# Kernel tuning notes

Measured on AMD Instinct MI355X. Metric: run time of the kernel, lower is better.

## Reference

```python
import jax, jax.numpy as jnp
import numpy as np

T, N, C, S = 1024, 128, 256, 64  # time, batch, classes, max label len
BLANK = 0
NEG = -1e30  # effective -inf that keeps logaddexp grads finite


def setup_inputs() -> dict:
    key = jax.random.key(0)
    k1, k2, k3 = jax.random.split(key, 3)
    logits = jax.random.normal(k1, (T, N, C), dtype=jnp.float32)
    y = jax.random.randint(k2, (N, S), 1, C)          # labels in [1, C), blank=0
    ylens = jax.random.randint(k3, (N, 1), 16, S + 1)  # 2*ylen+1 <= T always
    xlens = jnp.full((N, 1), T, dtype=jnp.int32)
    return {"logits": logits, "y": y, "xlens": xlens, "ylens": ylens}


def _ctc_loss(log_probs, y, xl, yl):
    """Standard CTC forward DP (alpha recursion), mean reduction, zero_infinity."""
    Tt, Nn, Cc = log_probs.shape
    Ss = y.shape[1]
    L = 2 * Ss + 1
    # extended label sequence: blank, y1, blank, y2, ..., blank
    ext = jnp.zeros((Nn, L), dtype=y.dtype).at[:, 1::2].set(y)
    # skip transition (s-2 -> s) allowed iff ext[s] != blank and ext[s] != ext[s-2]
    allow_skip = jnp.concatenate(
        [jnp.zeros((Nn, 2), bool),
         (ext[:, 2:] != ext[:, :-2]) & (ext[:, 2:] != BLANK)], axis=1)
    # gather per-time log-probs of extended labels: (T, N, L)
    lp_ext = jnp.take_along_axis(
        log_probs, jnp.broadcast_to(ext[None], (Tt, Nn, L)), axis=2)

    alpha0 = (jnp.full((Nn, L), NEG, jnp.float32)
              .at[:, 0].set(lp_ext[0, :, 0])
              .at[:, 1].set(lp_ext[0, :, 1]))

    def step(alpha, inp):
        lp_t, t = inp
        a1 = jnp.concatenate([jnp.full((Nn, 1), NEG, alpha.dtype), alpha[:, :-1]], axis=1)
        a2 = jnp.concatenate([jnp.full((Nn, 2), NEG, alpha.dtype), alpha[:, :-2]], axis=1)
        a2 = jnp.where(allow_skip, a2, NEG)
        new = lp_t + jnp.logaddexp(jnp.logaddexp(alpha, a1), a2)
        alpha = jnp.where((t < xl)[:, None], new, alpha)  # freeze past xlen
        return alpha, None

    alpha, _ = jax.lax.scan(step, alpha0, (lp_ext[1:], jnp.arange(1, Tt)))

    end = 2 * yl  # index of last blank in extended sequence
    la = jnp.take_along_axis(alpha, end[:, None], axis=1)[:, 0]
    lb = jnp.take_along_axis(alpha, (end - 1)[:, None], axis=1)[:, 0]
    nll = -jnp.logaddexp(la, lb)
    nll = jnp.where(jnp.isfinite(nll) & (nll < 1e29), nll, 0.0)  # zero_infinity
    return jnp.mean(nll / yl)  # reduction='mean': divide by target length, avg over batch


def reference(logits, y, xlens, ylens):
    log_probs = jax.nn.log_softmax(logits, axis=-1)
    return _ctc_loss(log_probs, y, xlens.reshape(-1), ylens.reshape(-1))
```

## Files before the change

kernel.cpp:

```cpp
#include <hip/hip_runtime.h>
#include <math.h>

constexpr int kT = 1024;
constexpr int kN = 128;
constexpr int kC = 256;
constexpr float NEGV = -1e30f;
constexpr int kRow = 260;
constexpr int kRowB = kRow * 4;
constexpr int kCH = 32;
constexpr int kNCH = 512 / kCH;
constexpr int kChF = 8 * kRow;
constexpr int kChB = kChF * 4;
constexpr float LOG2E = 1.4426950408889634f;
constexpr float LN2 = 0.6931471805599453f;

#if __has_builtin(__builtin_amdgcn_exp2f)
#define EXP2(x) __builtin_amdgcn_exp2f(x)
#else
#define EXP2(x) exp2f(x)
#endif
#if __has_builtin(__builtin_amdgcn_logf)
#define LOG2(x) __builtin_amdgcn_logf(x)
#else
#define LOG2(x) log2f(x)
#endif

struct TrueT { static constexpr bool value = true; };
struct FalseT { static constexpr bool value = false; };

__device__ __forceinline__ float lse2_2(float a, float b) {
    const float m = fmaxf(a, b);
    const float d = fminf(a, b) - m;
    return m + LOG2(1.0f + EXP2(d));
}

__device__ __forceinline__ float lse2_e(float a, float b) {
    const float m = fmaxf(a, b);
    return m + __logf(1.0f + __expf(fminf(a, b) - m));
}

__device__ __forceinline__ float lse3_e(float a, float b, float c) {
    const float m = fmaxf(fmaxf(a, b), c);
    return m + __logf(__expf(a - m) + __expf(b - m) + __expf(c - m));
}

template <bool GATHER>
__global__ __launch_bounds__(256) void k_lse(const float* __restrict__ logits,
                                             const int* __restrict__ y,
                                             float* __restrict__ lpg,
                                             float* __restrict__ lse_out) {
    __shared__ float srow[4][kC];
    __shared__ float sT[4][65];
    const int w = threadIdx.x >> 6;
    const int lane = threadIdx.x & 63;
    const int n = blockIdx.x & (kN - 1);
    const int t4 = blockIdx.x >> 7;
    const int t = t4 * 4 + w;
    const int row = t * kN + n;

    const float4 v = reinterpret_cast<const float4*>(logits + (size_t)row * kC)[lane];
    float m = fmaxf(fmaxf(v.x, v.y), fmaxf(v.z, v.w));
#pragma unroll
    for (int o = 32; o > 0; o >>= 1) m = fmaxf(m, __shfl_xor(m, o));
    float s = __expf(v.x - m) + __expf(v.y - m) + __expf(v.z - m) + __expf(v.w - m);
#pragma unroll
    for (int o = 32; o > 0; o >>= 1) s += __shfl_xor(s, o);

    if (GATHER) {
        const float log2s = LOG2(s);
        float* sr = srow[w];
        reinterpret_cast<float4*>(sr)[lane] = v;
        const int cls = y[(n << 6) + lane];
        sT[w][1 + lane] = (sr[cls] - m) * LOG2E - log2s;
        if (lane == 0) sT[w][0] = (v.x - m) * LOG2E - log2s;
        __syncthreads();
        float* op = lpg + (size_t)n * (kT / 4) * kRow + (size_t)t4 * kRow;
        const int tid = threadIdx.x;
        op[tid] = sT[tid & 3][tid >> 2];
        if (tid < 4) op[256 + tid] = sT[tid][64];
    } else {
        if (lane == 0) lse_out[row] = m + __logf(s);
    }
}

template <bool FRZ>
__device__ __forceinline__ void dp_step(float& A, float& B, float& C,
                                        float lpb, float lpy, bool skip,
                                        int lgrp, int l, bool commit) {
    const int bi = __float_as_int(B);
    const int b15 = __builtin_amdgcn_readlane(bi, 15);
    const int b31 = __builtin_amdgcn_readlane(bi, 31);
    const int b47 = __builtin_amdgcn_readlane(bi, 47);
    const int b63 = __builtin_amdgcn_readlane(bi, 63);
    const int bndi = (lgrp == 0) ? b63 : (lgrp == 1) ? b15 : (lgrp == 2) ? b31 : b47;
    const float am1 = __int_as_float(__builtin_amdgcn_update_dpp(
        bndi, bi, 0x111 , 0xF, 0xF, false));
    const float am1s = skip ? am1 : NEGV;
    const float x = fmaxf(B, A), yv = fminf(B, A);
    const float mB = fmaxf(x, am1s);
    const float dB1 = fmaxf(yv, fminf(x, am1s)) - mB;
    const float dB2 = fminf(yv, am1s) - mB;
    const float nB = (lpy + mB) + LOG2(1.0f + (EXP2(dB1) + EXP2(dB2)));
    const float u = (l == 0) ? C : A;
    const float mA = fmaxf(u, am1);
    const float lseA = mA + LOG2(1.0f + EXP2(fminf(u, am1) - mA));
    const float nA = lpb + ((l == 0) ? A : lseA);
    const float nC = lpb + lseA;
    if (FRZ) {
        A = commit ? nA : A;
        B = commit ? nB : B;
        C = commit ? nC : C;
    } else {
        A = nA; B = nB; C = nC;
    }
}

__global__ __launch_bounds__(512) void k_dp_split(const float* __restrict__ lpg,
                                                  const int* __restrict__ y,
                                                  const int* __restrict__ xlens,
                                                  const int* __restrict__ ylens,
                                                  float* __restrict__ nll_out) {
    __shared__ alignas(16) float sbf[2][kChF];
    __shared__ alignas(16) float sbb[2][kChF];
    __shared__ float st_f[130];
    __shared__ float st_b[130];
    const int n = blockIdx.x;
    const int wid = threadIdx.x >> 6;
    const int l = threadIdx.x & 63;
    const int lgrp = l >> 4;
    const char* src = (const char*)(lpg + (size_t)n * (kT / 4) * kRow);

    auto stage = [&](int c, int b, bool isF) {
        const int widx = isF ? (wid - 2) : (wid - 5);
        const long off = isF ? (long)c * kChB : (long)(256 - 8 * (c + 1)) * kRowB;
        const char* gs = src + off;
        char* ls = (char*)(isF ? &sbf[b][0] : &sbb[b][0]);
#pragma unroll
        for (int r = 0; r < 3; ++r) {
            const int wi = widx * 64 + r * 192;
            if (wi + l < kChB / 16) {
                __builtin_amdgcn_global_load_lds(
                    (const __attribute__((address_space(1))) void*)(gs + (size_t)(wi + l) * 16),
                    (__attribute__((address_space(3))) void*)(ls + (size_t)wi * 16), 16, 0, 0);
            }
        }
    };

    if (wid >= 2) stage(0, 0, wid < 5);
    __syncthreads();

    const int yl = ylens[n];
    const int xl = xlens[n];

    if (wid == 0) {
        const int ycur = y[(n << 6) + l];
        const int yprev = __shfl_up(ycur, 1);
        const bool skip = (l >= 1) && (ycur != yprev);
        float aA = (l == 0) ? sbf[0][0] : NEGV;
        float aB = (l == 0) ? sbf[0][4] : NEGV;
        float aC = NEGV;

        for (int c = 0; c < kNCH; ++c) {
            const float* B = sbf[c & 1];
            const int tb0 = c * kCH;
            auto body = [&](auto frzc) {
                constexpr bool FRZV = decltype(frzc)::value;
                float pb[2][4][4], py[2][4][4];
#define LOADF(H, D)                                                          \
    do {                                                                     \
        _Pragma("unroll") for (int q_ = 0; q_ < 4; ++q_) {                   \
            const int rb_ = (4 * (H) + q_) * kRow;                           \
            const float4 t0_ = *(const float4*)&B[rb_];                      \
            const float4 t1_ = *(const float4*)&B[rb_ + 4 + 4 * l];          \
            pb[D][q_][0] = t0_.x; pb[D][q_][1] = t0_.y;                      \
            pb[D][q_][2] = t0_.z; pb[D][q_][3] = t0_.w;                      \
            py[D][q_][0] = t1_.x; py[D][q_][1] = t1_.y;                      \
            py[D][q_][2] = t1_.z; py[D][q_][3] = t1_.w;                      \
        }                                                                    \
    } while (0)
                LOADF(0, 0);
#pragma unroll
                for (int h = 0; h < 2; ++h) {
                    const int cur = h & 1, nxt = cur ^ 1;
                    if (h < 1) LOADF(1, 1);
#pragma unroll
                    for (int q = 0; q < 4; ++q) {
#pragma unroll
                        for (int j = 0; j < 4; ++j) {
                            const int t = tb0 + 16 * h + 4 * q + j;
                            dp_step<FRZV>(aA, aB, aC, pb[cur][q][j], py[cur][q][j],
                                          skip, lgrp, l, (t > 0) & (t < xl));
                        }
                    }
                }
#undef LOADF
            };
            if (c == 0 || xl < 512) body(TrueT{});
            else body(FalseT{});
            __syncthreads();
        }
        st_f[2 * l] = aA;
        st_f[2 * l + 1] = aB;
        if (l == 0) st_f[128] = aC;
        __syncthreads();

        const float v0 = st_f[l] + st_b[l];
        const float v1 = st_f[64 + l] + st_b[64 + l];
        const float v2 = (l == 0) ? (st_f[128] + st_b[128]) : NEGV;
        float mm = fmaxf(fmaxf(v0, v1), v2);
#pragma unroll
        for (int o = 32; o > 0; o >>= 1) mm = fmaxf(mm, __shfl_xor(mm, o));
        float sm = EXP2(v0 - mm) + EXP2(v1 - mm) + EXP2(v2 - mm);
#pragma unroll
        for (int o = 32; o > 0; o >>= 1) sm += __shfl_xor(sm, o);
        if (l == 0) {
            float nll;
            if (xl <= 512) {
                nll = -lse2_2(st_f[2 * yl], st_f[2 * yl - 1]) * LN2;
            } else {
                nll = -(mm + LOG2(sm)) * LN2;
            }
            if (!(isfinite(nll) && nll < 1e29f)) nll = 0.0f;
            nll_out[n] = nll / (float)yl;
        }
    } else if (wid == 1) {
        const int ycb = y[(n << 6) + 63 - l];
        const int yup = __shfl_up(ycb, 1);
        const bool skipb = (l >= 1) && (ycb != yup);
        const int ls = 64 - yl;
        float bA = NEGV, bB = NEGV, b0 = NEGV;

        for (int c = 0; c < kNCH; ++c) {
            const float* B = sbb[c & 1];
            const int ttop = 1023 - kCH * c;
            auto body = [&](auto frzc) {
                constexpr bool FRZV = decltype(frzc)::value;
                float pb[2][4][4], py[2][4][4];
#define LOADB(H, D)                                                          \
    do {                                                                     \
        _Pragma("unroll") for (int q_ = 0; q_ < 4; ++q_) {                   \
            const int rb_ = (7 - 4 * (H) - q_) * kRow;                       \
            const float4 t0_ = *(const float4*)&B[rb_];                      \
            const float4 t1_ = *(const float4*)&B[rb_ + 256 - 4 * l];        \
            pb[D][q_][0] = t0_.x; pb[D][q_][1] = t0_.y;                      \
            pb[D][q_][2] = t0_.z; pb[D][q_][3] = t0_.w;                      \
            py[D][q_][0] = t1_.x; py[D][q_][1] = t1_.y;                      \
            py[D][q_][2] = t1_.z; py[D][q_][3] = t1_.w;                      \
        }                                                                    \
    } while (0)
                LOADB(0, 0);
#pragma unroll
                for (int h = 0; h < 2; ++h) {
                    const int cur = h & 1, nxt = cur ^ 1;
                    if (h < 1) LOADB(1, 1);
#pragma unroll
                    for (int q = 0; q < 4; ++q) {
#pragma unroll
                        for (int jr = 0; jr < 4; ++jr) {
                            const int j = 3 - jr;
                            const int t = ttop - (16 * h + 4 * q + jr);
                            const float lpb = pb[cur][q][j];
                            const float lpy = py[cur][q][j];
                            dp_step<FRZV>(bA, bB, b0, lpb, lpy, skipb, lgrp, l,
                                          (t >= 512) & (t <= xl - 2));
                            if (FRZV) {
                                const bool ss = (t == xl - 1);
                                bA = ss ? ((l == ls) ? lpb : NEGV) : bA;
                                bB = ss ? ((l == ls) ? lpy : NEGV) : bB;
                                b0 = ss ? NEGV : b0;
                            }
                        }
                    }
                }
#undef LOADB
            };
            if (c == 0 || xl < kT) body(TrueT{});
            else body(FalseT{});
            __syncthreads();
        }
        dp_step<false>(bA, bB, b0, 0.0f, 0.0f, skipb, lgrp, l, true);
        st_b[128 - 2 * l] = bA;
        st_b[127 - 2 * l] = bB;
        if (l == 0) st_b[0] = b0;
        __syncthreads();
    } else {
        for (int c = 0; c < kNCH; ++c) {
            if (c + 1 < kNCH) stage(c + 1, (c + 1) & 1, wid < 5);
            __syncthreads();
        }
        __syncthreads();
    }
}

template <int PFB>
__global__ __launch_bounds__(64) void k_dp_fb(const float* __restrict__ logits,
                                              const float* __restrict__ lsearr,
                                              const int* __restrict__ y,
                                              const int* __restrict__ xlens,
                                              const int* __restrict__ ylens,
                                              float* __restrict__ nll_out) {
    const int n = blockIdx.x;
    const int l = threadIdx.x;
    const int yl = ylens[n];
    const int xl = xlens[n];
    const int ycur = y[(n << 6) + l];
    const int yprev = __shfl_up(ycur, 1);
    const bool skip = (l >= 1) && (ycur != yprev);

    auto load_lp = [&](int t, float& lpb, float& lpy) {
        const float* p = logits + ((size_t)t * kN + n) * kC;
        const float d = lsearr[t * kN + n];
        lpb = p[0] - d;
        lpy = p[ycur] - d;
    };

    float lpb0, lpy0;
    load_lp(0, lpb0, lpy0);
    float aA = (l == 0) ? lpb0 : NEGV;
    float aB = (l == 0) ? lpy0 : NEGV;
    float aC = NEGV;

    float pb[PFB], py[PFB];
#pragma unroll
    for (int k = 0; k < PFB; ++k) load_lp(1 + k, pb[k], py[k]);

    for (int tb = 1; tb < kT; tb += PFB) {
#pragma unroll
        for (int k = 0; k < PFB; ++k) {
            const int t = tb + k;
            if (t < kT) {
                const float lpb = pb[k], lpy = py[k];
                if (t + PFB < kT) load_lp(t + PFB, pb[k], py[k]);
                float am1 = __shfl_up(aB, 1);
                if (l == 0) am1 = NEGV;
                const float nA = lpb + lse2_e(aA, am1);
                const float nB = lpy + lse3_e(aB, aA, skip ? am1 : NEGV);
                float nC = aC;
                if (l == 63) nC = lpb + lse2_e(aC, aB);
                if (t < xl) { aA = nA; aB = nB; aC = nC; }
            }
        }
    }

    __shared__ float st[130];
    st[2 * l] = aA;
    st[2 * l + 1] = aB;
    if (l == 63) st[128] = aC;
    __syncthreads();
    if (l == 0) {
        const int end = 2 * yl;
        float nll = -lse2_e(st[end], st[end - 1]);
        if (!(isfinite(nll) && nll < 1e29f)) nll = 0.0f;
        nll_out[n] = nll / (float)yl;
    }
}

__global__ __launch_bounds__(128) void k_reduce(const float* __restrict__ nll,
                                                float* __restrict__ out) {
    const int tid = threadIdx.x;
    float v = nll[tid];
#pragma unroll
    for (int o = 32; o > 0; o >>= 1) v += __shfl_xor(v, o);
    __shared__ float partial[2];
    if ((tid & 63) == 0) partial[tid >> 6] = v;
    __syncthreads();
    if (tid == 0) out[0] = (partial[0] + partial[1]) * (1.0f / (float)kN);
}

extern "C" void kernel_launch(void* const* d_in, const int* in_sizes, int n_in,
                              void* d_out, int out_size, void* d_ws, size_t ws_size,
                              hipStream_t stream) {
    const float* logits = (const float*)d_in[0];
    const int* y = (const int*)d_in[1];
    const int* xlens = (const int*)d_in[2];
    const int* ylens = (const int*)d_in[3];
    float* out = (float*)d_out;

    const size_t need_full =
        (size_t)kN * (kT / 4) * kRow * sizeof(float) + kN * sizeof(float);
    const int rows = kT * kN;

    if (ws_size >= need_full) {
        float* lpg = (float*)d_ws;
        float* nll = lpg + (size_t)kN * (kT / 4) * kRow;
        k_lse<true><<<rows / 4, 256, 0, stream>>>(logits, y, lpg, nullptr);
        k_dp_split<<<kN, 512, 0, stream>>>(lpg, y, xlens, ylens, nll);
        k_reduce<<<1, kN, 0, stream>>>(nll, out);
    } else {
        float* lsearr = (float*)d_ws;
        float* nll = lsearr + (size_t)rows;
        k_lse<false><<<rows / 4, 256, 0, stream>>>(logits, y, nullptr, lsearr);
        k_dp_fb<8><<<kN, 64, 0, stream>>>(logits, lsearr, y, xlens, ylens, nll);
        k_reduce<<<1, kN, 0, stream>>>(nll, out);
    }
}
```

Baseline: 96.20 us.

## Fuse log-softmax gather into DP kernel producer warps

Removes the separate log-softmax/gather kernel and its workspace intermediate; producer warps in the DP kernel now load logits rows directly, compute the row max and sum via wave shuffles, gather the label log-probs through shared scratch, and write them into the double-buffered LDS chunks. This avoids a kernel launch and a global write/read of the gathered array. The trade-off is that all logits traffic now comes from only 128 blocks, which may cut achievable bandwidth, and the producer compute must keep pace with the serial DP warps. The low-workspace fallback path is dropped.

```diff
diff --git a/kernel.cpp b/kernel.cpp
--- a/kernel.cpp
+++ b/kernel.cpp
@@ -6,11 +6,9 @@
 constexpr int kC = 256;
 constexpr float NEGV = -1e30f;
 constexpr int kRow = 260;
-constexpr int kRowB = kRow * 4;
 constexpr int kCH = 32;
 constexpr int kNCH = 512 / kCH;
 constexpr int kChF = 8 * kRow;
-constexpr int kChB = kChF * 4;
 constexpr float LOG2E = 1.4426950408889634f;
 constexpr float LN2 = 0.6931471805599453f;
 
@@ -32,55 +30,6 @@
     const float m = fmaxf(a, b);
     const float d = fminf(a, b) - m;
     return m + LOG2(1.0f + EXP2(d));
-}
-
-__device__ __forceinline__ float lse2_e(float a, float b) {
-    const float m = fmaxf(a, b);
-    return m + __logf(1.0f + __expf(fminf(a, b) - m));
-}
-
-__device__ __forceinline__ float lse3_e(float a, float b, float c) {
-    const float m = fmaxf(fmaxf(a, b), c);
-    return m + __logf(__expf(a - m) + __expf(b - m) + __expf(c - m));
-}
-
-template <bool GATHER>
-__global__ __launch_bounds__(256) void k_lse(const float* __restrict__ logits,
-                                             const int* __restrict__ y,
-                                             float* __restrict__ lpg,
-                                             float* __restrict__ lse_out) {
-    __shared__ float srow[4][kC];
-    __shared__ float sT[4][65];
-    const int w = threadIdx.x >> 6;
-    const int lane = threadIdx.x & 63;
-    const int n = blockIdx.x & (kN - 1);
-    const int t4 = blockIdx.x >> 7;
-    const int t = t4 * 4 + w;
-    const int row = t * kN + n;
-
-    const float4 v = reinterpret_cast<const float4*>(logits + (size_t)row * kC)[lane];
-    float m = fmaxf(fmaxf(v.x, v.y), fmaxf(v.z, v.w));
-#pragma unroll
-    for (int o = 32; o > 0; o >>= 1) m = fmaxf(m, __shfl_xor(m, o));
-    float s = __expf(v.x - m) + __expf(v.y - m) + __expf(v.z - m) + __expf(v.w - m);
-#pragma unroll
-    for (int o = 32; o > 0; o >>= 1) s += __shfl_xor(s, o);
-
-    if (GATHER) {
-        const float log2s = LOG2(s);
-        float* sr = srow[w];
-        reinterpret_cast<float4*>(sr)[lane] = v;
-        const int cls = y[(n << 6) + lane];
-        sT[w][1 + lane] = (sr[cls] - m) * LOG2E - log2s;
-        if (lane == 0) sT[w][0] = (v.x - m) * LOG2E - log2s;
-        __syncthreads();
-        float* op = lpg + (size_t)n * (kT / 4) * kRow + (size_t)t4 * kRow;
-        const int tid = threadIdx.x;
-        op[tid] = sT[tid & 3][tid >> 2];
-        if (tid < 4) op[256 + tid] = sT[tid][64];
-    } else {
-        if (lane == 0) lse_out[row] = m + __logf(s);
-    }
 }
 
 template <bool FRZ>
@@ -115,47 +64,74 @@
     }
 }
 
-__global__ __launch_bounds__(512) void k_dp_split(const float* __restrict__ lpg,
-                                                  const int* __restrict__ y,
-                                                  const int* __restrict__ xlens,
-                                                  const int* __restrict__ ylens,
-                                                  float* __restrict__ nll_out) {
+__global__ __launch_bounds__(512) void k_ctc_fused(const float* __restrict__ logits,
+                                                   const int* __restrict__ y,
+                                                   const int* __restrict__ xlens,
+                                                   const int* __restrict__ ylens,
+                                                   float* __restrict__ nll_out) {
     __shared__ alignas(16) float sbf[2][kChF];
     __shared__ alignas(16) float sbb[2][kChF];
+    __shared__ alignas(16) float scr[6][kC];
     __shared__ float st_f[130];
     __shared__ float st_b[130];
     const int n = blockIdx.x;
     const int wid = threadIdx.x >> 6;
     const int l = threadIdx.x & 63;
     const int lgrp = l >> 4;
-    const char* src = (const char*)(lpg + (size_t)n * (kT / 4) * kRow);
-
-    auto stage = [&](int c, int b, bool isF) {
-        const int widx = isF ? (wid - 2) : (wid - 5);
-        const long off = isF ? (long)c * kChB : (long)(256 - 8 * (c + 1)) * kRowB;
-        const char* gs = src + off;
-        char* ls = (char*)(isF ? &sbf[b][0] : &sbb[b][0]);
-#pragma unroll
-        for (int r = 0; r < 3; ++r) {
-            const int wi = widx * 64 + r * 192;
-            if (wi + l < kChB / 16) {
-                __builtin_amdgcn_global_load_lds(
-                    (const __attribute__((address_space(1))) void*)(gs + (size_t)(wi + l) * 16),
-                    (__attribute__((address_space(3))) void*)(ls + (size_t)wi * 16), 16, 0, 0);
-            }
-        }
-    };
-
-    if (wid >= 2) stage(0, 0, wid < 5);
-    __syncthreads();
 
     const int yl = ylens[n];
     const int xl = xlens[n];
+    const int cls = y[(n << 6) + l];
+
+    auto stage_sm = [&](int c, bool isF, float* dst) {
+        const int widx = isF ? (wid - 2) : (wid - 5);
+        const int scrw = wid - 2;
+        float4 v0, v1, v2, v3, v4, v5, v6, v7, v8, v9, v10;
+#define ROWT(K) (isF ? (c * kCH + widx + 3 * (K)) : (992 - kCH * c + widx + 3 * (K)))
+#define LOADR(K, V)                                                           \
+    do {                                                                      \
+        if (widx + 3 * (K) < kCH) {                                           \
+            const int tg_ = ROWT(K);                                          \
+            V = *reinterpret_cast<const float4*>(                             \
+                logits + ((size_t)tg_ * kN + n) * kC + 4 * l);                \
+        }                                                                     \
+    } while (0)
+        LOADR(0, v0); LOADR(1, v1); LOADR(2, v2); LOADR(3, v3);
+        LOADR(4, v4); LOADR(5, v5); LOADR(6, v6); LOADR(7, v7);
+        LOADR(8, v8); LOADR(9, v9); LOADR(10, v10);
+#define PROCR(K, V)                                                           \
+    do {                                                                      \
+        const int r_ = widx + 3 * (K);                                        \
+        if (r_ < kCH) {                                                       \
+            float m_ = fmaxf(fmaxf(V.x, V.y), fmaxf(V.z, V.w));               \
+            _Pragma("unroll") for (int o_ = 32; o_ > 0; o_ >>= 1)             \
+                m_ = fmaxf(m_, __shfl_xor(m_, o_));                           \
+            float s_ = __expf(V.x - m_) + __expf(V.y - m_) +                  \
+                       __expf(V.z - m_) + __expf(V.w - m_);                   \
+            _Pragma("unroll") for (int o_ = 32; o_ > 0; o_ >>= 1)             \
+                s_ += __shfl_xor(s_, o_);                                     \
+            const float l2s_ = LOG2(s_);                                      \
+            reinterpret_cast<float4*>(&scr[scrw][0])[l] = V;                  \
+            const float g_ = scr[scrw][cls];                                  \
+            const int t4_ = r_ >> 2, j_ = r_ & 3;                             \
+            dst[t4_ * kRow + (1 + l) * 4 + j_] = (g_ - m_) * LOG2E - l2s_;    \
+            if (l == 0) dst[t4_ * kRow + j_] = (V.x - m_) * LOG2E - l2s_;     \
+        }                                                                     \
+    } while (0)
+        PROCR(0, v0); PROCR(1, v1); PROCR(2, v2); PROCR(3, v3);
+        PROCR(4, v4); PROCR(5, v5); PROCR(6, v6); PROCR(7, v7);
+        PROCR(8, v8); PROCR(9, v9); PROCR(10, v10);
+#undef PROCR
+#undef LOADR
+#undef ROWT
+    };
+
+    if (wid >= 2) stage_sm(0, wid < 5, (wid < 5) ? sbf[0] : sbb[0]);
+    __syncthreads();
 
     if (wid == 0) {
-        const int ycur = y[(n << 6) + l];
-        const int yprev = __shfl_up(ycur, 1);
-        const bool skip = (l >= 1) && (ycur != yprev);
+        const int yprev = __shfl_up(cls, 1);
+        const bool skip = (l >= 1) && (cls != yprev);
         float aA = (l == 0) ? sbf[0][0] : NEGV;
         float aB = (l == 0) ? sbf[0][4] : NEGV;
         float aC = NEGV;
@@ -181,7 +157,7 @@
                 LOADF(0, 0);
 #pragma unroll
                 for (int h = 0; h < 2; ++h) {
-                    const int cur = h & 1, nxt = cur ^ 1;
+                    const int cur = h & 1;
                     if (h < 1) LOADF(1, 1);
 #pragma unroll
                     for (int q = 0; q < 4; ++q) {
@@ -251,7 +227,7 @@
                 LOADB(0, 0);
 #pragma unroll
                 for (int h = 0; h < 2; ++h) {
-                    const int cur = h & 1, nxt = cur ^ 1;
+                    const int cur = h & 1;
                     if (h < 1) LOADB(1, 1);
 #pragma unroll
                     for (int q = 0; q < 4; ++q) {
@@ -284,74 +260,13 @@
         if (l == 0) st_b[0] = b0;
         __syncthreads();
     } else {
+        const bool isF = wid < 5;
         for (int c = 0; c < kNCH; ++c) {
-            if (c + 1 < kNCH) stage(c + 1, (c + 1) & 1, wid < 5);
+            if (c + 1 < kNCH)
+                stage_sm(c + 1, isF, isF ? sbf[(c + 1) & 1] : sbb[(c + 1) & 1]);
             __syncthreads();
         }
         __syncthreads();
-    }
-}
-
-template <int PFB>
-__global__ __launch_bounds__(64) void k_dp_fb(const float* __restrict__ logits,
-                                              const float* __restrict__ lsearr,
-                                              const int* __restrict__ y,
-                                              const int* __restrict__ xlens,
-                                              const int* __restrict__ ylens,
-                                              float* __restrict__ nll_out) {
-    const int n = blockIdx.x;
-    const int l = threadIdx.x;
-    const int yl = ylens[n];
-    const int xl = xlens[n];
-    const int ycur = y[(n << 6) + l];
-    const int yprev = __shfl_up(ycur, 1);
-    const bool skip = (l >= 1) && (ycur != yprev);
-
-    auto load_lp = [&](int t, float& lpb, float& lpy) {
-        const float* p = logits + ((size_t)t * kN + n) * kC;
-        const float d = lsearr[t * kN + n];
-        lpb = p[0] - d;
-        lpy = p[ycur] - d;
-    };
-
-    float lpb0, lpy0;
-    load_lp(0, lpb0, lpy0);
-    float aA = (l == 0) ? lpb0 : NEGV;
-    float aB = (l == 0) ? lpy0 : NEGV;
-    float aC = NEGV;
-
-    float pb[PFB], py[PFB];
-#pragma unroll
-    for (int k = 0; k < PFB; ++k) load_lp(1 + k, pb[k], py[k]);
-
-    for (int tb = 1; tb < kT; tb += PFB) {
-#pragma unroll
-        for (int k = 0; k < PFB; ++k) {
-            const int t = tb + k;
-            if (t < kT) {
-                const float lpb = pb[k], lpy = py[k];
-                if (t + PFB < kT) load_lp(t + PFB, pb[k], py[k]);
-                float am1 = __shfl_up(aB, 1);
-                if (l == 0) am1 = NEGV;
-                const float nA = lpb + lse2_e(aA, am1);
-                const float nB = lpy + lse3_e(aB, aA, skip ? am1 : NEGV);
-                float nC = aC;
-                if (l == 63) nC = lpb + lse2_e(aC, aB);
-                if (t < xl) { aA = nA; aB = nB; aC = nC; }
-            }
-        }
-    }
-
-    __shared__ float st[130];
-    st[2 * l] = aA;
-    st[2 * l + 1] = aB;
-    if (l == 63) st[128] = aC;
-    __syncthreads();
-    if (l == 0) {
-        const int end = 2 * yl;
-        float nll = -lse2_e(st[end], st[end - 1]);
-        if (!(isfinite(nll) && nll < 1e29f)) nll = 0.0f;
-        nll_out[n] = nll / (float)yl;
     }
 }
 
@@ -376,21 +291,7 @@
     const int* ylens = (const int*)d_in[3];
     float* out = (float*)d_out;
 
-    const size_t need_full =
-        (size_t)kN * (kT / 4) * kRow * sizeof(float) + kN * sizeof(float);
-    const int rows = kT * kN;
-
-    if (ws_size >= need_full) {
-        float* lpg = (float*)d_ws;
-        float* nll = lpg + (size_t)kN * (kT / 4) * kRow;
-        k_lse<true><<<rows / 4, 256, 0, stream>>>(logits, y, lpg, nullptr);
-        k_dp_split<<<kN, 512, 0, stream>>>(lpg, y, xlens, ylens, nll);
-        k_reduce<<<1, kN, 0, stream>>>(nll, out);
-    } else {
-        float* lsearr = (float*)d_ws;
-        float* nll = lsearr + (size_t)rows;
-        k_lse<false><<<rows / 4, 256, 0, stream>>>(logits, y, nullptr, lsearr);
-        k_dp_fb<8><<<kN, 64, 0, stream>>>(logits, lsearr, y, xlens, ylens, nll);
-        k_reduce<<<1, kN, 0, stream>>>(nll, out);
-    }
-}
+    float* nll = (float*)d_ws;
+    k_ctc_fused<<<kN, 512, 0, stream>>>(logits, y, xlens, ylens, nll);
+    k_reduce<<<1, kN, 0, stream>>>(nll, out);
+}
```

After: 113.9 us. +18.4%, slower.

## Fuse two CTC DP time steps into one windowed transition per iteration

Applied to the files above, without the earlier changes.

The forward and backward alpha/beta recursions now advance two time steps per iteration in unfrozen chunks. A precomputed two-step transition (win_step) combines the log-probs of both steps into combined edge weights, so each pair of steps needs one log-sum-exp per state instead of two chained ones. This halves the serial dependency chain of DPP shifts and log/exp operations. In exchange it adds extra LDS loads for the neighbour's log-prob, more cross-lane shifts and more exp terms per step, and the rearranged sum order may change floating-point results slightly.

```diff
diff --git a/kernel.cpp b/kernel.cpp
--- a/kernel.cpp
+++ b/kernel.cpp
@@ -26,7 +26,6 @@
 #endif
 
 struct TrueT { static constexpr bool value = true; };
-struct FalseT { static constexpr bool value = false; };
 
 __device__ __forceinline__ float lse2_2(float a, float b) {
     const float m = fmaxf(a, b);
@@ -83,18 +82,21 @@
     }
 }
 
+__device__ __forceinline__ float row_shr1_b(float x, int lgrp) {
+    const int xi = __float_as_int(x);
+    const int b15 = __builtin_amdgcn_readlane(xi, 15);
+    const int b31 = __builtin_amdgcn_readlane(xi, 31);
+    const int b47 = __builtin_amdgcn_readlane(xi, 47);
+    const int b63 = __builtin_amdgcn_readlane(xi, 63);
+    const int bnd = (lgrp == 0) ? b63 : (lgrp == 1) ? b15 : (lgrp == 2) ? b31 : b47;
+    return __int_as_float(__builtin_amdgcn_update_dpp(bnd, xi, 0x111, 0xF, 0xF, false));
+}
+
 template <bool FRZ>
 __device__ __forceinline__ void dp_step(float& A, float& B, float& C,
                                         float lpb, float lpy, bool skip,
                                         int lgrp, int l, bool commit) {
-    const int bi = __float_as_int(B);
-    const int b15 = __builtin_amdgcn_readlane(bi, 15);
-    const int b31 = __builtin_amdgcn_readlane(bi, 31);
-    const int b47 = __builtin_amdgcn_readlane(bi, 47);
-    const int b63 = __builtin_amdgcn_readlane(bi, 63);
-    const int bndi = (lgrp == 0) ? b63 : (lgrp == 1) ? b15 : (lgrp == 2) ? b31 : b47;
-    const float am1 = __int_as_float(__builtin_amdgcn_update_dpp(
-        bndi, bi, 0x111 , 0xF, 0xF, false));
+    const float am1 = row_shr1_b(B, lgrp);
     const float am1s = skip ? am1 : NEGV;
     const float x = fmaxf(B, A), yv = fminf(B, A);
     const float mB = fmaxf(x, am1s);
@@ -115,6 +117,42 @@
     }
 }
 
+__device__ __forceinline__ void win_step(float& A, float& B, float& C,
+                                         float lpb0, float lpy0, float lpb1,
+                                         float lpy1, float lpy0m1, float skf,
+                                         float skm1f, float og2, float og4,
+                                         float e3g, int lgrp, int l) {
+    const float E0 = lpb0 + lpb1;
+    const float E1 = lpb1 + lse2_2(lpb0, lpy0m1);
+    const float E2 = lpb1 + lpy0m1;
+    const float E3 = E2 + skm1f + e3g;
+    const float O0 = lpy1 + lpy0;
+    const float O1 = lpy1 + lse2_2(lpy0, lpb0);
+    const float p0 = lpb0, p1 = skf + lpy0m1, p2 = skf + lpy0;
+    const float mx = fmaxf(fmaxf(p0, p1), p2);
+    const float md = fmaxf(fminf(p0, p1), fminf(fmaxf(p0, p1), p2));
+    const float mn = fminf(fminf(p0, p1), p2);
+    const float O2 = lpy1 + og2 + (mx + LOG2(1.0f + EXP2(md - mx) + EXP2(mn - mx)));
+    const float O3 = lpy1 + og2 + skf + lpy0m1;
+    const float O4 = lpy1 + og4 + skf + skm1f + lpy0m1;
+    const float s1A = row_shr1_b(A, lgrp);
+    const float s1B = row_shr1_b(B, lgrp);
+    const float s2B = row_shr1_b(s1B, lgrp);
+    const float u = (l == 0) ? C : A;
+    const float q0 = E0 + u, q1 = E1 + s1B, q2 = E2 + s1A, q3 = E3 + s2B;
+    const float mE = fmaxf(fmaxf(q0, q1), fmaxf(q2, q3));
+    const float sE = (EXP2(q0 - mE) + EXP2(q1 - mE)) + (EXP2(q2 - mE) + EXP2(q3 - mE));
+    const float lseE = mE + LOG2(sE);
+    const float nA = (l == 0) ? (E0 + A) : lseE;
+    const float nC = lseE;
+    const float r0 = O0 + B, r1 = O1 + A, r2 = O2 + s1B, r3 = O3 + s1A, r4 = O4 + s2B;
+    const float mO = fmaxf(fmaxf(fmaxf(r0, r1), fmaxf(r2, r3)), r4);
+    const float sO = (EXP2(r0 - mO) + EXP2(r1 - mO)) +
+                     (EXP2(r2 - mO) + EXP2(r3 - mO)) + EXP2(r4 - mO);
+    const float nB = mO + LOG2(sO);
+    A = nA; B = nB; C = nC;
+}
+
 __global__ __launch_bounds__(512) void k_dp_split(const float* __restrict__ lpg,
                                                   const int* __restrict__ y,
                                                   const int* __restrict__ xlens,
@@ -151,11 +189,18 @@
 
     const int yl = ylens[n];
     const int xl = xlens[n];
+    const float og2 = (l >= 1) ? 0.0f : NEGV;
+    const float og4 = (l >= 2) ? 0.0f : NEGV;
+    const float e3g = (l == 1) ? NEGV : 0.0f;
 
     if (wid == 0) {
         const int ycur = y[(n << 6) + l];
         const int yprev = __shfl_up(ycur, 1);
         const bool skip = (l >= 1) && (ycur != yprev);
+        const float skf = skip ? 0.0f : NEGV;
+        const float skm1f = __shfl(skf, (l + 63) & 63);
+        const int im1f = (l == 0) ? 256 : 4 * l;
+
         float aA = (l == 0) ? sbf[0][0] : NEGV;
         float aB = (l == 0) ? sbf[0][4] : NEGV;
         float aC = NEGV;
@@ -163,8 +208,7 @@
         for (int c = 0; c < kNCH; ++c) {
             const float* B = sbf[c & 1];
             const int tb0 = c * kCH;
-            auto body = [&](auto frzc) {
-                constexpr bool FRZV = decltype(frzc)::value;
+            if (c == 0 || tb0 + kCH - 1 >= xl) {
                 float pb[2][4][4], py[2][4][4];
 #define LOADF(H, D)                                                          \
     do {                                                                     \
@@ -181,22 +225,51 @@
                 LOADF(0, 0);
 #pragma unroll
                 for (int h = 0; h < 2; ++h) {
-                    const int cur = h & 1, nxt = cur ^ 1;
                     if (h < 1) LOADF(1, 1);
 #pragma unroll
                     for (int q = 0; q < 4; ++q) {
 #pragma unroll
                         for (int j = 0; j < 4; ++j) {
                             const int t = tb0 + 16 * h + 4 * q + j;
-                            dp_step<FRZV>(aA, aB, aC, pb[cur][q][j], py[cur][q][j],
+                            dp_step<true>(aA, aB, aC, pb[h][q][j], py[h][q][j],
                                           skip, lgrp, l, (t > 0) & (t < xl));
                         }
                     }
                 }
 #undef LOADF
-            };
-            if (c == 0 || xl < 512) body(TrueT{});
-            else body(FalseT{});
+            } else {
+                float pb[2][4][4], py[2][4][4], ph[2][4][4];
+#define LOADW(H, D)                                                          \
+    do {                                                                     \
+        _Pragma("unroll") for (int q_ = 0; q_ < 4; ++q_) {                   \
+            const int rb_ = (4 * (H) + q_) * kRow;                           \
+            const float4 t0_ = *(const float4*)&B[rb_];                      \
+            const float4 t1_ = *(const float4*)&B[rb_ + 4 + 4 * l];          \
+            const float4 t2_ = *(const float4*)&B[rb_ + im1f];               \
+            pb[D][q_][0] = t0_.x; pb[D][q_][1] = t0_.y;                      \
+            pb[D][q_][2] = t0_.z; pb[D][q_][3] = t0_.w;                      \
+            py[D][q_][0] = t1_.x; py[D][q_][1] = t1_.y;                      \
+            py[D][q_][2] = t1_.z; py[D][q_][3] = t1_.w;                      \
+            ph[D][q_][0] = t2_.x; ph[D][q_][1] = t2_.y;                      \
+            ph[D][q_][2] = t2_.z; ph[D][q_][3] = t2_.w;                      \
+        }                                                                    \
+    } while (0)
+                LOADW(0, 0);
+#pragma unroll
+                for (int h = 0; h < 2; ++h) {
+                    if (h < 1) LOADW(1, 1);
+#pragma unroll
+                    for (int q = 0; q < 4; ++q) {
+                        win_step(aA, aB, aC, pb[h][q][0], py[h][q][0],
+                                 pb[h][q][1], py[h][q][1], ph[h][q][0], skf,
+                                 skm1f, og2, og4, e3g, lgrp, l);
+                        win_step(aA, aB, aC, pb[h][q][2], py[h][q][2],
+                                 pb[h][q][3], py[h][q][3], ph[h][q][2], skf,
+                                 skm1f, og2, og4, e3g, lgrp, l);
+                    }
+                }
+#undef LOADW
+            }
             __syncthreads();
         }
         st_f[2 * l] = aA;
@@ -227,14 +300,16 @@
         const int ycb = y[(n << 6) + 63 - l];
         const int yup = __shfl_up(ycb, 1);
         const bool skipb = (l >= 1) && (ycb != yup);
+        const float skf = skipb ? 0.0f : NEGV;
+        const float skm1f = __shfl(skf, (l + 63) & 63);
+        const int im1b = (l == 0) ? 4 : 260 - 4 * l;
         const int ls = 64 - yl;
         float bA = NEGV, bB = NEGV, b0 = NEGV;
 
         for (int c = 0; c < kNCH; ++c) {
             const float* B = sbb[c & 1];
             const int ttop = 1023 - kCH * c;
-            auto body = [&](auto frzc) {
-                constexpr bool FRZV = decltype(frzc)::value;
+            if (ttop >= xl - 1) {
                 float pb[2][4][4], py[2][4][4];
 #define LOADB(H, D)                                                          \
     do {                                                                     \
@@ -251,7 +326,6 @@
                 LOADB(0, 0);
 #pragma unroll
                 for (int h = 0; h < 2; ++h) {
-                    const int cur = h & 1, nxt = cur ^ 1;
                     if (h < 1) LOADB(1, 1);
 #pragma unroll
                     for (int q = 0; q < 4; ++q) {
@@ -259,23 +333,51 @@
                         for (int jr = 0; jr < 4; ++jr) {
                             const int j = 3 - jr;
                             const int t = ttop - (16 * h + 4 * q + jr);
-                            const float lpb = pb[cur][q][j];
-                            const float lpy = py[cur][q][j];
-                            dp_step<FRZV>(bA, bB, b0, lpb, lpy, skipb, lgrp, l,
+                            const float lpb = pb[h][q][j];
+                            const float lpy = py[h][q][j];
+                            dp_step<true>(bA, bB, b0, lpb, lpy, skipb, lgrp, l,
                                           (t >= 512) & (t <= xl - 2));
-                            if (FRZV) {
-                                const bool ss = (t == xl - 1);
-                                bA = ss ? ((l == ls) ? lpb : NEGV) : bA;
-                                bB = ss ? ((l == ls) ? lpy : NEGV) : bB;
-                                b0 = ss ? NEGV : b0;
-                            }
+                            const bool ss = (t == xl - 1);
+                            bA = ss ? ((l == ls) ? lpb : NEGV) : bA;
+                            bB = ss ? ((l == ls) ? lpy : NEGV) : bB;
+                            b0 = ss ? NEGV : b0;
                         }
                     }
                 }
 #undef LOADB
-            };
-            if (c == 0 || xl < kT) body(TrueT{});
-            else body(FalseT{});
+            } else {
+                float pb[2][4][4], py[2][4][4], ph[2][4][4];
+#define LOADWB(H, D)                                                         \
+    do {                                                                     \
+        _Pragma("unroll") for (int q_ = 0; q_ < 4; ++q_) {                   \
+            const int rb_ = (7 - 4 * (H) - q_) * kRow;                       \
+            const float4 t0_ = *(const float4*)&B[rb_];                      \
+            const float4 t1_ = *(const float4*)&B[rb_ + 256 - 4 * l];        \
+            const float4 t2_ = *(const float4*)&B[rb_ + im1b];               \
+            pb[D][q_][0] = t0_.x; pb[D][q_][1] = t0_.y;                      \
+            pb[D][q_][2] = t0_.z; pb[D][q_][3] = t0_.w;                      \
+            py[D][q_][0] = t1_.x; py[D][q_][1] = t1_.y;                      \
+            py[D][q_][2] = t1_.z; py[D][q_][3] = t1_.w;                      \
+            ph[D][q_][0] = t2_.x; ph[D][q_][1] = t2_.y;                      \
+            ph[D][q_][2] = t2_.z; ph[D][q_][3] = t2_.w;                      \
+        }                                                                    \
+    } while (0)
+                LOADWB(0, 0);
+#pragma unroll
+                for (int h = 0; h < 2; ++h) {
+                    if (h < 1) LOADWB(1, 1);
+#pragma unroll
+                    for (int q = 0; q < 4; ++q) {
+                        win_step(bA, bB, b0, pb[h][q][3], py[h][q][3],
+                                 pb[h][q][2], py[h][q][2], ph[h][q][3], skf,
+                                 skm1f, og2, og4, e3g, lgrp, l);
+                        win_step(bA, bB, b0, pb[h][q][1], py[h][q][1],
+                                 pb[h][q][0], py[h][q][0], ph[h][q][1], skf,
+                                 skm1f, og2, og4, e3g, lgrp, l);
+                    }
+                }
+#undef LOADWB
+            }
             __syncthreads();
         }
         dp_step<false>(bA, bB, b0, 0.0f, 0.0f, skipb, lgrp, l, true);
@@ -284,8 +386,9 @@
         if (l == 0) st_b[0] = b0;
         __syncthreads();
     } else {
+        const bool isF = wid < 5;
         for (int c = 0; c < kNCH; ++c) {
-            if (c + 1 < kNCH) stage(c + 1, (c + 1) & 1, wid < 5);
+            if (c + 1 < kNCH) stage(c + 1, (c + 1) & 1, isF);
             __syncthreads();
         }
         __syncthreads();
```

Result: slower. 123.4 us (+28.3%).

## Replace log-space CTC recursion with mantissa/exponent scaled linear-space DP

Applied to the files above, without the earlier changes.

The gather kernel now stores linear-domain probabilities (exp(x-m)/s) instead of log2 probabilities. The forward and backward alpha/beta recursions keep each state as an integer exponent plus a float mantissa. Additions use ldexp alignment and multiplications by the probabilities, with frexp for renormalisation, replacing the exp2/log2 transcendental calls in every step. This removes the per-step transcendental cost but adds integer max, ldexp and frexp work, DPP shifts on two registers, and the risk of underflow when aligning small terms.

```diff
diff --git a/kernel.cpp b/kernel.cpp
--- a/kernel.cpp
+++ b/kernel.cpp
@@ -11,7 +11,7 @@
 constexpr int kNCH = 512 / kCH;
 constexpr int kChF = 8 * kRow;
 constexpr int kChB = kChF * 4;
-constexpr float LOG2E = 1.4426950408889634f;
+constexpr int SENT = -(1 << 28);
 constexpr float LN2 = 0.6931471805599453f;
 
 #if __has_builtin(__builtin_amdgcn_exp2f)
@@ -24,6 +24,28 @@
 #else
 #define LOG2(x) log2f(x)
 #endif
+
+__device__ __forceinline__ float fxm(float x) {
+#if __has_builtin(__builtin_amdgcn_frexp_mantf)
+    return __builtin_amdgcn_frexp_mantf(x);
+#else
+    int e; return frexpf(x, &e);
+#endif
+}
+__device__ __forceinline__ int fxe(float x) {
+#if __has_builtin(__builtin_amdgcn_frexp_expf)
+    return __builtin_amdgcn_frexp_expf(x);
+#else
+    int e; frexpf(x, &e); return e;
+#endif
+}
+__device__ __forceinline__ float ldx(float x, int e) {
+#if __has_builtin(__builtin_amdgcn_ldexpf)
+    return __builtin_amdgcn_ldexpf(x, e);
+#else
+    return ldexpf(x, e);
+#endif
+}
 
 struct TrueT { static constexpr bool value = true; };
 struct FalseT { static constexpr bool value = false; };
@@ -67,12 +89,12 @@
     for (int o = 32; o > 0; o >>= 1) s += __shfl_xor(s, o);
 
     if (GATHER) {
-        const float log2s = LOG2(s);
+        const float rs = 1.0f / s;
         float* sr = srow[w];
         reinterpret_cast<float4*>(sr)[lane] = v;
         const int cls = y[(n << 6) + lane];
-        sT[w][1 + lane] = (sr[cls] - m) * LOG2E - log2s;
-        if (lane == 0) sT[w][0] = (v.x - m) * LOG2E - log2s;
+        sT[w][1 + lane] = __expf(sr[cls] - m) * rs;
+        if (lane == 0) sT[w][0] = __expf(v.x - m) * rs;
         __syncthreads();
         float* op = lpg + (size_t)n * (kT / 4) * kRow + (size_t)t4 * kRow;
         const int tid = threadIdx.x;
@@ -83,36 +105,54 @@
     }
 }
 
+__device__ __forceinline__ int row_shr1_i(int xi, int lgrp) {
+    const int b15 = __builtin_amdgcn_readlane(xi, 15);
+    const int b31 = __builtin_amdgcn_readlane(xi, 31);
+    const int b47 = __builtin_amdgcn_readlane(xi, 47);
+    const int b63 = __builtin_amdgcn_readlane(xi, 63);
+    const int bnd = (lgrp == 0) ? b63 : (lgrp == 1) ? b15 : (lgrp == 2) ? b31 : b47;
+    return __builtin_amdgcn_update_dpp(bnd, xi, 0x111, 0xF, 0xF, false);
+}
+__device__ __forceinline__ float row_shr1_f(float x, int lgrp) {
+    return __int_as_float(row_shr1_i(__float_as_int(x), lgrp));
+}
+
 template <bool FRZ>
-__device__ __forceinline__ void dp_step(float& A, float& B, float& C,
-                                        float lpb, float lpy, bool skip,
-                                        int lgrp, int l, bool commit) {
-    const int bi = __float_as_int(B);
-    const int b15 = __builtin_amdgcn_readlane(bi, 15);
-    const int b31 = __builtin_amdgcn_readlane(bi, 31);
-    const int b47 = __builtin_amdgcn_readlane(bi, 47);
-    const int b63 = __builtin_amdgcn_readlane(bi, 63);
-    const int bndi = (lgrp == 0) ? b63 : (lgrp == 1) ? b15 : (lgrp == 2) ? b31 : b47;
-    const float am1 = __int_as_float(__builtin_amdgcn_update_dpp(
-        bndi, bi, 0x111 , 0xF, 0xF, false));
-    const float am1s = skip ? am1 : NEGV;
-    const float x = fmaxf(B, A), yv = fminf(B, A);
-    const float mB = fmaxf(x, am1s);
-    const float dB1 = fmaxf(yv, fminf(x, am1s)) - mB;
-    const float dB2 = fminf(yv, am1s) - mB;
-    const float nB = (lpy + mB) + LOG2(1.0f + (EXP2(dB1) + EXP2(dB2)));
-    const float u = (l == 0) ? C : A;
-    const float mA = fmaxf(u, am1);
-    const float lseA = mA + LOG2(1.0f + EXP2(fminf(u, am1) - mA));
-    const float nA = lpb + ((l == 0) ? A : lseA);
-    const float nC = lpb + lseA;
+__device__ __forceinline__ void ms_step(int& mA, float& sA, int& mB, float& sB,
+                                        int& mC, float& sC, float Pb, float Py,
+                                        bool skip, int lgrp, int l, bool commit) {
+    const int m1 = row_shr1_i(mB, lgrp);
+    const float s1 = row_shr1_f(sB, lgrp);
+    const int msk = skip ? m1 : SENT;
+    const int p = max(max(mB, mA), msk);
+    const float tB = ldx(sB, mB - p);
+    const float tA = ldx(sA, mA - p);
+    const float tS = ldx(s1, msk - p);
+    const float v = Py * ((tB + tA) + tS);
+    const int nmB = p + fxe(v);
+    const float nsB = fxm(v);
+    const int um = (l == 0) ? mC : mA;
+    const float us = (l == 0) ? sC : sA;
+    const int q = max(um, m1);
+    const float w = Pb * (ldx(us, um - q) + ldx(s1, m1 - q));
+    const int mE = q + fxe(w);
+    const float sE = fxm(w);
+    const float w0 = Pb * sA;
+    const int nmA = (l == 0) ? (mA + fxe(w0)) : mE;
+    const float nsA = (l == 0) ? fxm(w0) : sE;
+    const int nmC = mE;
+    const float nsC = sE;
     if (FRZ) {
-        A = commit ? nA : A;
-        B = commit ? nB : B;
-        C = commit ? nC : C;
+        mA = commit ? nmA : mA; sA = commit ? nsA : sA;
+        mB = commit ? nmB : mB; sB = commit ? nsB : sB;
+        mC = commit ? nmC : mC; sC = commit ? nsC : sC;
     } else {
-        A = nA; B = nB; C = nC;
-    }
+        mA = nmA; sA = nsA; mB = nmB; sB = nsB; mC = nmC; sC = nsC;
+    }
+}
+
+__device__ __forceinline__ float ms2log(int m, float s) {
+    return (s > 0.0f) ? ((float)m + LOG2(s)) : NEGV;
 }
 
 __global__ __launch_bounds__(512) void k_dp_split(const float* __restrict__ lpg,
@@ -156,9 +196,13 @@
         const int ycur = y[(n << 6) + l];
         const int yprev = __shfl_up(ycur, 1);
         const bool skip = (l >= 1) && (ycur != yprev);
-        float aA = (l == 0) ? sbf[0][0] : NEGV;
-        float aB = (l == 0) ? sbf[0][4] : NEGV;
-        float aC = NEGV;
+        const float P0b = sbf[0][0], P0y = sbf[0][4];
+        int mA = (l == 0) ? fxe(P0b) : SENT;
+        float sA = (l == 0) ? fxm(P0b) : 0.0f;
+        int mB = (l == 0) ? fxe(P0y) : SENT;
+        float sB = (l == 0) ? fxm(P0y) : 0.0f;
+        int mC = SENT;
+        float sC = 0.0f;
 
         for (int c = 0; c < kNCH; ++c) {
             const float* B = sbf[c & 1];
@@ -181,15 +225,15 @@
                 LOADF(0, 0);
 #pragma unroll
                 for (int h = 0; h < 2; ++h) {
-                    const int cur = h & 1, nxt = cur ^ 1;
                     if (h < 1) LOADF(1, 1);
 #pragma unroll
                     for (int q = 0; q < 4; ++q) {
 #pragma unroll
                         for (int j = 0; j < 4; ++j) {
                             const int t = tb0 + 16 * h + 4 * q + j;
-                            dp_step<FRZV>(aA, aB, aC, pb[cur][q][j], py[cur][q][j],
-                                          skip, lgrp, l, (t > 0) & (t < xl));
+                            ms_step<FRZV>(mA, sA, mB, sB, mC, sC, pb[h][q][j],
+                                          py[h][q][j], skip, lgrp, l,
+                                          (t > 0) & (t < xl));
                         }
                     }
                 }
@@ -199,9 +243,9 @@
             else body(FalseT{});
             __syncthreads();
         }
-        st_f[2 * l] = aA;
-        st_f[2 * l + 1] = aB;
-        if (l == 0) st_f[128] = aC;
+        st_f[2 * l] = ms2log(mA, sA);
+        st_f[2 * l + 1] = ms2log(mB, sB);
+        if (l == 0) st_f[128] = ms2log(mC, sC);
         __syncthreads();
 
         const float v0 = st_f[l] + st_b[l];
@@ -228,7 +272,8 @@
         const int yup = __shfl_up(ycb, 1);
         const bool skipb = (l >= 1) && (ycb != yup);
         const int ls = 64 - yl;
-        float bA = NEGV, bB = NEGV, b0 = NEGV;
+        int mA = SENT, mB = SENT, m0 = SENT;
+        float sA = 0.0f, sB = 0.0f, s0 = 0.0f;
 
         for (int c = 0; c < kNCH; ++c) {
             const float* B = sbb[c & 1];
@@ -251,7 +296,6 @@
                 LOADB(0, 0);
 #pragma unroll
                 for (int h = 0; h < 2; ++h) {
-                    const int cur = h & 1, nxt = cur ^ 1;
                     if (h < 1) LOADB(1, 1);
 #pragma unroll
                     for (int q = 0; q < 4; ++q) {
@@ -259,15 +303,19 @@
                         for (int jr = 0; jr < 4; ++jr) {
                             const int j = 3 - jr;
                             const int t = ttop - (16 * h + 4 * q + jr);
-                            const float lpb = pb[cur][q][j];
-                            const float lpy = py[cur][q][j];
-                            dp_step<FRZV>(bA, bB, b0, lpb, lpy, skipb, lgrp, l,
-                                          (t >= 512) & (t <= xl - 2));
+                            const float Pb = pb[h][q][j];
+                            const float Py = py[h][q][j];
+                            ms_step<FRZV>(mA, sA, mB, sB, m0, s0, Pb, Py, skipb,
+                                          lgrp, l, (t >= 512) & (t <= xl - 2));
                             if (FRZV) {
                                 const bool ss = (t == xl - 1);
-                                bA = ss ? ((l == ls) ? lpb : NEGV) : bA;
-                                bB = ss ? ((l == ls) ? lpy : NEGV) : bB;
-                                b0 = ss ? NEGV : b0;
+                                const bool sl = ss & (l == ls);
+                                mA = ss ? (sl ? fxe(Pb) : SENT) : mA;
+                                sA = ss ? (sl ? fxm(Pb) : 0.0f) : sA;
+                                mB = ss ? (sl ? fxe(Py) : SENT) : mB;
+                                sB = ss ? (sl ? fxm(Py) : 0.0f) : sB;
+                                m0 = ss ? SENT : m0;
+                                s0 = ss ? 0.0f : s0;
                             }
                         }
                     }
@@ -278,14 +326,15 @@
             else body(FalseT{});
             __syncthreads();
         }
-        dp_step<false>(bA, bB, b0, 0.0f, 0.0f, skipb, lgrp, l, true);
-        st_b[128 - 2 * l] = bA;
-        st_b[127 - 2 * l] = bB;
-        if (l == 0) st_b[0] = b0;
+        ms_step<false>(mA, sA, mB, sB, m0, s0, 1.0f, 1.0f, skipb, lgrp, l, true);
+        st_b[128 - 2 * l] = ms2log(mA, sA);
+        st_b[127 - 2 * l] = ms2log(mB, sB);
+        if (l == 0) st_b[0] = ms2log(m0, s0);
         __syncthreads();
     } else {
+        const bool isF = wid < 5;
         for (int c = 0; c < kNCH; ++c) {
-            if (c + 1 < kNCH) stage(c + 1, (c + 1) & 1, wid < 5);
+            if (c + 1 < kNCH) stage(c + 1, (c + 1) & 1, isF);
             __syncthreads();
         }
         __syncthreads();
```

Measured after the change: 117.8 us. +22.4%, slower.
